# Kernel tuning notes

Measured on AMD Instinct MI355X. Metric: run time of the kernel, lower is better.

## Reference

```python
import jax, jax.numpy as jnp
import numpy as np

B, S, D = 4, 2048, 1024  # batch, seq_len, isize; FFN hidden = isize, gate dim = 2*isize


def setup_inputs() -> dict:
    key = jax.random.key(0)
    ks = jax.random.split(key, 6)
    sc = lambda n: 1.0 / np.sqrt(n)
    return {
        "iQ": jax.random.normal(ks[0], (B, S, D), jnp.float32),
        "iV": jax.random.normal(ks[1], (B, S, D), jnp.float32),
        "W1": jax.random.normal(ks[2], (D, D), jnp.float32) * sc(D),
        "b1": jnp.zeros((D,), jnp.float32),
        "W2": jax.random.normal(ks[3], (D, D), jnp.float32) * sc(D),
        "b2": jnp.zeros((D,), jnp.float32),
        "Wg": jax.random.normal(ks[4], (2 * D, 2 * D), jnp.float32) * sc(2 * D),
        "bg": jnp.zeros((2 * D,), jnp.float32),
    }


def reference(iQ, iV, W1, b1, W2, b2, Wg, bg):
    seql = iV.shape[1]
    # AAN cumulative-average matrix: row i has 1/(i+1) in cols 0..i (lower triangular)
    inv = 1.0 / jnp.arange(1, seql + 1, dtype=iV.dtype)  # [S]
    attn = jnp.tril(jnp.broadcast_to(inv[:, None], (seql, seql)))  # [S, S]
    avg = jnp.einsum('st,btd->bsd', attn, iV)  # [B, S, D]
    # PositionwiseFF with norm_input=False, dropout=0: Linear -> ReLU -> Linear
    h = jax.nn.relu(avg @ W1 + b1)
    ffn = h @ W2 + b2  # [B, S, D]
    # sigmoid gate over concat(iQ, ffn)
    g = jax.nn.sigmoid(jnp.concatenate([iQ, ffn], axis=-1) @ Wg + bg)  # [B, S, 2D]
    d = ffn.shape[-1]
    igate = g[..., :d]
    fgate = g[..., d:]
    return igate * iQ + fgate * ffn
```

## Files before the change

### kernel.cpp

```cpp
#include <hip/hip_runtime.h>
#include <hip/hip_bf16.h>
#include <cstdint>

typedef unsigned short u16;
typedef unsigned int   u32;

typedef __attribute__((ext_vector_type(8))) short short8;
typedef __attribute__((ext_vector_type(4))) float f32x4;

__device__ __forceinline__ float b2f(u16 v) { return __uint_as_float(((u32)v) << 16); }
__device__ __forceinline__ u16 f2b(float f) {
    u32 u = __float_as_uint(f);
    u += 0x7FFFu + ((u >> 16) & 1u);
    return (u16)(u >> 16);
}

#define G2L16(gp, lp) __builtin_amdgcn_global_load_lds(                       \
    (const __attribute__((address_space(1))) void*)(gp),                      \
    (__attribute__((address_space(3))) void*)(lp), 16, 0, 0)

__device__ __forceinline__ void transpose_body(const float* __restrict__ in,
                                               u16* __restrict__ out,
                                               int R, int C, int lb, int tilesX,
                                               float (*tile)[33]) {
    const int bx = (lb % tilesX) * 32;
    const int by = (lb / tilesX) * 32;
    const int tx = threadIdx.x & 31, ty = threadIdx.x >> 5;
    #pragma unroll
    for (int i = 0; i < 32; i += 8)
        tile[ty + i][tx] = in[(size_t)(by + ty + i) * C + (bx + tx)];
    __syncthreads();
    #pragma unroll
    for (int i = 0; i < 32; i += 8)
        out[(size_t)(bx + ty + i) * R + (by + tx)] = f2b(tile[tx][ty + i]);
}

__global__ void prologue_kernel(const float* __restrict__ W1, u16* __restrict__ W1t,
                                const float* __restrict__ W2, u16* __restrict__ W2t,
                                const float* __restrict__ Wg, u16* __restrict__ Wgt,
                                const float* __restrict__ iQ, u16* __restrict__ iQb,
                                const float* __restrict__ iV, float* __restrict__ csum) {
    __shared__ float tile[32][33];
    const int bid = blockIdx.x;
    const int tid = threadIdx.x;
    if (bid < 1024) {
        transpose_body(W1, W1t, 1024, 1024, bid, 32, tile);
    } else if (bid < 2048) {
        transpose_body(W2, W2t, 1024, 1024, bid - 1024, 32, tile);
    } else if (bid < 6144) {
        transpose_body(Wg, Wgt, 2048, 2048, bid - 2048, 64, tile);
    } else if (bid < 14336) {
        const size_t i = ((size_t)(bid - 6144) * 256 + tid) * 4;
        const float4 v = *(const float4*)(iQ + i);
        ushort4 o;
        o.x = f2b(v.x); o.y = f2b(v.y); o.z = f2b(v.z); o.w = f2b(v.w);
        *(ushort4*)(iQb + i) = o;
    } else {
        const int idx = bid - 14336;
        const int b = idx >> 6, c = idx & 63;
        const int d = tid * 4;
        const float* src = iV + ((size_t)(b * 2048 + c * 32)) * 1024 + d;
        float4 s = {0.f, 0.f, 0.f, 0.f};
        #pragma unroll 8
        for (int i = 0; i < 32; ++i) {
            const float4 v = *(const float4*)(src + (size_t)i * 1024);
            s.x += v.x; s.y += v.y; s.z += v.z; s.w += v.w;
        }
        *(float4*)(csum + ((size_t)(b * 64 + c)) * 1024 + d) = s;
    }
}

__global__ void scan_kernel(const float* __restrict__ iV, const float* __restrict__ csum,
                            u16* __restrict__ avg) {
    const int c = blockIdx.x & 63, b = blockIdx.x >> 6;
    const int d = threadIdx.x * 4;
    const float* cs = csum + (size_t)b * 64 * 1024 + d;
    float4 a0 = {0,0,0,0}, a1 = {0,0,0,0}, a2 = {0,0,0,0}, a3 = {0,0,0,0};
    int cc = 0;
    for (; cc + 4 <= c; cc += 4) {
        const float4 v0 = *(const float4*)(cs + (size_t)(cc + 0) * 1024);
        const float4 v1 = *(const float4*)(cs + (size_t)(cc + 1) * 1024);
        const float4 v2 = *(const float4*)(cs + (size_t)(cc + 2) * 1024);
        const float4 v3 = *(const float4*)(cs + (size_t)(cc + 3) * 1024);
        a0.x += v0.x; a0.y += v0.y; a0.z += v0.z; a0.w += v0.w;
        a1.x += v1.x; a1.y += v1.y; a1.z += v1.z; a1.w += v1.w;
        a2.x += v2.x; a2.y += v2.y; a2.z += v2.z; a2.w += v2.w;
        a3.x += v3.x; a3.y += v3.y; a3.z += v3.z; a3.w += v3.w;
    }
    for (; cc < c; ++cc) {
        const float4 v = *(const float4*)(cs + (size_t)cc * 1024);
        a0.x += v.x; a0.y += v.y; a0.z += v.z; a0.w += v.w;
    }
    float4 acc;
    acc.x = (a0.x + a1.x) + (a2.x + a3.x);
    acc.y = (a0.y + a1.y) + (a2.y + a3.y);
    acc.z = (a0.z + a1.z) + (a2.z + a3.z);
    acc.w = (a0.w + a1.w) + (a2.w + a3.w);

    const size_t off = ((size_t)(b * 2048 + c * 32)) * 1024 + d;
    const float* src = iV + off;
    u16*         dst = avg + off;
    const int s0 = c * 32;
    #pragma unroll 4
    for (int i = 0; i < 32; ++i) {
        const float4 v = *(const float4*)(src + (size_t)i * 1024);
        acc.x += v.x; acc.y += v.y; acc.z += v.z; acc.w += v.w;
        const float inv = 1.0f / (float)(s0 + i + 1);
        ushort4 o;
        o.x = f2b(acc.x * inv); o.y = f2b(acc.y * inv);
        o.z = f2b(acc.z * inv); o.w = f2b(acc.w * inv);
        *(ushort4*)(dst + (size_t)i * 1024) = o;
    }
}

template <int EPI>
__global__ __launch_bounds__(256, 2)
void gemm_kernel(const u16* __restrict__ A, const u16* __restrict__ Bt,
                 const float* __restrict__ bias, u16* __restrict__ C,
                 int M, int N, int K) {
    __shared__ u16 As[128 * 64];
    __shared__ u16 Bs[128 * 64];

    const int tid  = threadIdx.x;
    const int m0   = blockIdx.x * 128;
    const int n0   = blockIdx.y * 128;
    const int wave = tid >> 6, lane = tid & 63;
    const int wm   = (wave & 1) << 6;
    const int wn   = (wave >> 1) << 6;
    const int quad = lane >> 4, l16 = lane & 15;

    f32x4 acc[4][4];
    #pragma unroll
    for (int i = 0; i < 4; ++i)
        #pragma unroll
        for (int j = 0; j < 4; ++j) acc[i][j] = (f32x4){0.f, 0.f, 0.f, 0.f};

    int oo[4], rr[4], qq[4];
    #pragma unroll
    for (int j = 0; j < 4; ++j) {
        oo[j] = tid * 16 + j * 4096;
        rr[j] = oo[j] >> 7;
        qq[j] = ((oo[j] >> 4) & 7) ^ (rr[j] & 7);
    }

    const int ktiles = K >> 6;
    for (int kt = 0; kt < ktiles; ++kt) {
        const int kb = kt << 6;
        #pragma unroll
        for (int j = 0; j < 4; ++j) {
            G2L16((const char*)A  + ((size_t)(m0 + rr[j]) * K + kb) * 2 + qq[j] * 16,
                  (char*)As + oo[j]);
            G2L16((const char*)Bt + ((size_t)(n0 + rr[j]) * K + kb) * 2 + qq[j] * 16,
                  (char*)Bs + oo[j]);
        }
        __syncthreads();

        #pragma unroll
        for (int h = 0; h < 2; ++h) {
            short8 af[4], bf[4];
            #pragma unroll
            for (int mi = 0; mi < 4; ++mi) {
                const int R = wm + mi * 16 + l16;
                af[mi] = *(const short8*)(As + R * 64 + ((((h << 2) | quad) ^ (R & 7)) << 3));
            }
            #pragma unroll
            for (int ni = 0; ni < 4; ++ni) {
                const int R = wn + ni * 16 + l16;
                bf[ni] = *(const short8*)(Bs + R * 64 + ((((h << 2) | quad) ^ (R & 7)) << 3));
            }
            #pragma unroll
            for (int mi = 0; mi < 4; ++mi)
                #pragma unroll
                for (int ni = 0; ni < 4; ++ni)
                    acc[mi][ni] = __builtin_amdgcn_mfma_f32_16x16x32_bf16(
                        af[mi], bf[ni], acc[mi][ni], 0, 0, 0);
        }
        __syncthreads();
    }

    #pragma unroll
    for (int ni = 0; ni < 4; ++ni) {
        const int col = n0 + wn + ni * 16 + l16;
        const float bv = bias[col];
        #pragma unroll
        for (int mi = 0; mi < 4; ++mi) {
            const int row0 = m0 + wm + mi * 16 + quad * 4;
            #pragma unroll
            for (int r = 0; r < 4; ++r) {
                float v = acc[mi][ni][r] + bv;
                if (EPI == 0) v = fmaxf(v, 0.f);
                C[(size_t)(row0 + r) * N + col] = f2b(v);
            }
        }
    }
}

#define VM4  asm volatile("s_waitcnt vmcnt(4)" ::: "memory")
#define VM0  asm volatile("s_waitcnt vmcnt(0)" ::: "memory")
#define NOVM ((void)0)

#define SA(BUF, MH, T) do {                                                     \
    const char* b_ = ((T) < 16) ? ((const char*)iQb + (size_t)(T) * 128)        \
                                : ((const char*)ffn + (size_t)((T) - 16) * 128); \
    G2L16(b_ + gA[MH][0], (char*)&As[BUF][MH][0] + lo[0]);                      \
    G2L16(b_ + gA[MH][1], (char*)&As[BUF][MH][0] + lo[1]);                      \
  } while (0)

#define SB(BUF, GG, T) do {                                                     \
    const char* b_ = (const char*)Wgt + (size_t)(T) * 128;                      \
    G2L16(b_ + gB[GG][0], (char*)&Bs[BUF][GG][0] + lo[0]);                      \
    G2L16(b_ + gB[GG][1], (char*)&Bs[BUF][GG][0] + lo[1]);                      \
  } while (0)

#define PHASE(BUF, MH, G, STAGES, VMW) do {                                     \
    short8 af[4][2], bf[2][2];                                                  \
    {                                                                           \
      const char* Ab_ = (const char*)&As[BUF][MH][0];                           \
      const char* Bb_ = (const char*)&Bs[BUF][G][0];                            \
      _Pragma("unroll")                                                         \
      for (int mi = 0; mi < 4; ++mi) {                                          \
        af[mi][0] = *(const short8*)(Ab_ + aF[mi][0]);                          \
        af[mi][1] = *(const short8*)(Ab_ + aF[mi][1]);                          \
      }                                                                         \
      bf[0][0] = *(const short8*)(Bb_ + bF[0][0]);                              \
      bf[0][1] = *(const short8*)(Bb_ + bF[0][1]);                              \
      bf[1][0] = *(const short8*)(Bb_ + bF[1][0]);                              \
      bf[1][1] = *(const short8*)(Bb_ + bF[1][1]);                              \
    }                                                                           \
    STAGES                                                                      \
    __builtin_amdgcn_sched_barrier(0);                                          \
    __builtin_amdgcn_s_barrier();                                               \
    asm volatile("s_waitcnt lgkmcnt(0)" ::: "memory");                          \
    __builtin_amdgcn_sched_barrier(0);                                          \
    __builtin_amdgcn_s_setprio(1);                                              \
    _Pragma("unroll")                                                           \
    for (int mi = 0; mi < 4; ++mi) {                                            \
      _Pragma("unroll")                                                         \
      for (int ni = 0; ni < 2; ++ni) {                                          \
        acc[G][(MH) * 4 + mi][ni] = __builtin_amdgcn_mfma_f32_16x16x32_bf16(    \
            af[mi][0], bf[ni][0], acc[G][(MH) * 4 + mi][ni], 0, 0, 0);          \
        acc[G][(MH) * 4 + mi][ni] = __builtin_amdgcn_mfma_f32_16x16x32_bf16(    \
            af[mi][1], bf[ni][1], acc[G][(MH) * 4 + mi][ni], 0, 0, 0);          \
      }                                                                         \
    }                                                                           \
    __builtin_amdgcn_s_setprio(0);                                              \
    __builtin_amdgcn_sched_barrier(0);                                          \
    VMW;                                                                        \
    __builtin_amdgcn_s_barrier();                                               \
    __builtin_amdgcn_sched_barrier(0);                                          \
  } while (0)

__global__ __launch_bounds__(512, 2)
void gate8_kernel(const u16* __restrict__ iQb, const u16* __restrict__ ffn,
                  const u16* __restrict__ Wgt, const float* __restrict__ bg,
                  const float* __restrict__ iQ, float* __restrict__ out) {
    __shared__ u16 As[2][2][128 * 64];
    __shared__ u16 Bs[2][2][128 * 64];

    const int tid  = threadIdx.x;
    const int bid  = blockIdx.x;
    const int m0   = (bid & 31) * 256;
    const int n0   = (bid >> 5) * 128;
    const int wave = tid >> 6, lane = tid & 63;
    const int wm   = wave & 1;
    const int wn   = wave >> 1;
    const int quad = lane >> 4, l16 = lane & 15;

    u32 lo[2], gA[2][2], gB[2][2];
    #pragma unroll
    for (int j = 0; j < 2; ++j) {
        const u32 o = (u32)tid * 16 + (u32)j * 8192;
        const u32 r = o >> 7;
        const u32 q = ((o >> 4) & 7) ^ (r & 7);
        lo[j]    = o;
        gA[0][j] = (u32)(m0 + r) * 2048 + q * 16;
        gA[1][j] = (u32)(m0 + 128 + r) * 2048 + q * 16;
        gB[0][j] = (u32)(n0 + r) * 4096 + q * 16;
        gB[1][j] = (u32)(n0 + 1024 + r) * 4096 + q * 16;
    }

    u32 aF[4][2], bF[2][2];
    #pragma unroll
    for (int mi = 0; mi < 4; ++mi) {
        const int R = wm * 64 + mi * 16 + l16;
        #pragma unroll
        for (int ks = 0; ks < 2; ++ks)
            aF[mi][ks] = (u32)R * 128 + (u32)((((ks << 2) | quad) ^ (R & 7)) << 4);
    }
    #pragma unroll
    for (int ni = 0; ni < 2; ++ni) {
        const int R = wn * 32 + ni * 16 + l16;
        #pragma unroll
        for (int ks = 0; ks < 2; ++ks)
            bF[ni][ks] = (u32)R * 128 + (u32)((((ks << 2) | quad) ^ (R & 7)) << 4);
    }

    f32x4 acc[2][8][2];
    #pragma unroll
    for (int g = 0; g < 2; ++g)
        #pragma unroll
        for (int mf = 0; mf < 8; ++mf)
            #pragma unroll
            for (int ni = 0; ni < 2; ++ni)
                acc[g][mf][ni] = (f32x4){0.f, 0.f, 0.f, 0.f};

    SA(0, 0, 0); SA(0, 1, 0); SB(0, 0, 0); SB(0, 1, 0);
    SA(1, 0, 1); SB(1, 1, 1);
    VM4;
    __builtin_amdgcn_s_barrier();
    __builtin_amdgcn_sched_barrier(0);

    for (int i = 0; i < 15; ++i) {
        const int t0 = 2 * i, t1 = t0 + 1;
        PHASE(0, 0, 0, SA(1, 1, t1);     SB(1, 0, t1);     , NOVM);
        PHASE(0, 0, 1,                                     , NOVM);
        PHASE(0, 1, 1, SA(0, 0, t0 + 2);                   , NOVM);
        PHASE(0, 1, 0, SB(0, 1, t0 + 2);                   , VM4);
        PHASE(1, 0, 0, SB(0, 0, t0 + 2); SA(0, 1, t0 + 2); , NOVM);
        PHASE(1, 0, 1,                                     , NOVM);
        PHASE(1, 1, 1, SA(1, 0, t1 + 2);                   , NOVM);
        PHASE(1, 1, 0, SB(1, 1, t1 + 2);                   , VM4);
    }
    PHASE(0, 0, 0, SA(1, 1, 31); SB(1, 0, 31); , NOVM);
    PHASE(0, 0, 1,                             , NOVM);
    PHASE(0, 1, 1,                             , NOVM);
    PHASE(0, 1, 0,                             , VM0);
    PHASE(1, 0, 0,                             , NOVM);
    PHASE(1, 0, 1,                             , NOVM);
    PHASE(1, 1, 1,                             , NOVM);
    PHASE(1, 1, 0,                             , NOVM);

    #pragma unroll
    for (int ni = 0; ni < 2; ++ni) {
        const int col = n0 + wn * 32 + ni * 16 + l16;
        const float bgi = bg[col];
        const float bgf = bg[col + 1024];
        #pragma unroll
        for (int mh = 0; mh < 2; ++mh)
            #pragma unroll
            for (int mi = 0; mi < 4; ++mi) {
                const int row0 = m0 + mh * 128 + wm * 64 + mi * 16 + quad * 4;
                #pragma unroll
                for (int r = 0; r < 4; ++r) {
                    const size_t idx = (size_t)(row0 + r) * 1024 + col;
                    const float gi = 1.0f / (1.0f + __expf(-(acc[0][mh * 4 + mi][ni][r] + bgi)));
                    const float gf = 1.0f / (1.0f + __expf(-(acc[1][mh * 4 + mi][ni][r] + bgf)));
                    out[idx] = gi * iQ[idx] + gf * b2f(ffn[idx]);
                }
            }
    }
}

extern "C" void kernel_launch(void* const* d_in, const int* in_sizes, int n_in,
                              void* d_out, int out_size, void* d_ws, size_t ws_size,
                              hipStream_t stream) {
    const int B = 4, S = 2048, D = 1024, D2 = 2048;
    const int M = B * S;

    const float* iQ = (const float*)d_in[0];
    const float* iV = (const float*)d_in[1];
    const float* W1 = (const float*)d_in[2];
    const float* b1 = (const float*)d_in[3];
    const float* W2 = (const float*)d_in[4];
    const float* b2 = (const float*)d_in[5];
    const float* Wg = (const float*)d_in[6];
    const float* bg = (const float*)d_in[7];
    float* out = (float*)d_out;

    u16*   regA = (u16*)d_ws;
    u16*   regB = regA + (size_t)M * D;
    u16*   iQb  = regB + (size_t)M * D;
    u16*   W1t  = iQb  + (size_t)M * D;
    u16*   W2t  = W1t  + (size_t)D * D;
    u16*   Wgt  = W2t  + (size_t)D * D;
    float* csum = (float*)(Wgt + (size_t)D2 * D2);

    u16* avg = regA;
    u16* ffn = regA;
    u16* h   = regB;

    prologue_kernel<<<14592, 256, 0, stream>>>(W1, W1t, W2, W2t, Wg, Wgt,
                                               iQ, iQb, iV, csum);
    scan_kernel<<<B * 64, 256, 0, stream>>>(iV, csum, avg);
    gemm_kernel<0><<<dim3(M / 128, D / 128), 256, 0, stream>>>(avg, W1t, b1, h, M, D, D);
    gemm_kernel<1><<<dim3(M / 128, D / 128), 256, 0, stream>>>(h, W2t, b2, ffn, M, D, D);
    gate8_kernel<<<256, 512, 0, stream>>>(iQb, ffn, Wgt, bg, iQ, out);
}
```

Measured before the change: 284.4 us.

## Restructure gate GEMM into four phases with both B-halves kept in registers

```diff
diff --git a/kernel.cpp b/kernel.cpp
--- a/kernel.cpp
+++ b/kernel.cpp
@@ -212,20 +212,27 @@
     G2L16(b_ + gB[GG][1], (char*)&Bs[BUF][GG][0] + lo[1]);                      \
   } while (0)
 
-#define PHASE(BUF, MH, G, STAGES, VMW) do {                                     \
-    short8 af[4][2], bf[2][2];                                                  \
+#define PHASE(BUF, MH, RDB, STAGES, VMW) do {                                   \
+    short8 af[4][2];                                                            \
     {                                                                           \
       const char* Ab_ = (const char*)&As[BUF][MH][0];                           \
-      const char* Bb_ = (const char*)&Bs[BUF][G][0];                            \
       _Pragma("unroll")                                                         \
       for (int mi = 0; mi < 4; ++mi) {                                          \
         af[mi][0] = *(const short8*)(Ab_ + aF[mi][0]);                          \
         af[mi][1] = *(const short8*)(Ab_ + aF[mi][1]);                          \
       }                                                                         \
-      bf[0][0] = *(const short8*)(Bb_ + bF[0][0]);                              \
-      bf[0][1] = *(const short8*)(Bb_ + bF[0][1]);                              \
-      bf[1][0] = *(const short8*)(Bb_ + bF[1][0]);                              \
-      bf[1][1] = *(const short8*)(Bb_ + bF[1][1]);                              \
+      if (RDB) {                                                                \
+        const char* B0_ = (const char*)&Bs[BUF][0][0];                          \
+        const char* B1_ = (const char*)&Bs[BUF][1][0];                          \
+        _Pragma("unroll")                                                       \
+        for (int ni = 0; ni < 2; ++ni) {                                        \
+          _Pragma("unroll")                                                     \
+          for (int ks = 0; ks < 2; ++ks) {                                      \
+            bf[0][ni][ks] = *(const short8*)(B0_ + bF[ni][ks]);                 \
+            bf[1][ni][ks] = *(const short8*)(B1_ + bF[ni][ks]);                 \
+          }                                                                     \
+        }                                                                       \
+      }                                                                         \
     }                                                                           \
     STAGES                                                                      \
     __builtin_amdgcn_sched_barrier(0);                                          \
@@ -234,13 +241,16 @@
     __builtin_amdgcn_sched_barrier(0);                                          \
     __builtin_amdgcn_s_setprio(1);                                              \
     _Pragma("unroll")                                                           \
-    for (int mi = 0; mi < 4; ++mi) {                                            \
+    for (int ks = 0; ks < 2; ++ks) {                                            \
       _Pragma("unroll")                                                         \
-      for (int ni = 0; ni < 2; ++ni) {                                          \
-        acc[G][(MH) * 4 + mi][ni] = __builtin_amdgcn_mfma_f32_16x16x32_bf16(    \
-            af[mi][0], bf[ni][0], acc[G][(MH) * 4 + mi][ni], 0, 0, 0);          \
-        acc[G][(MH) * 4 + mi][ni] = __builtin_amdgcn_mfma_f32_16x16x32_bf16(    \
-            af[mi][1], bf[ni][1], acc[G][(MH) * 4 + mi][ni], 0, 0, 0);          \
+      for (int mi = 0; mi < 4; ++mi) {                                          \
+        _Pragma("unroll")                                                       \
+        for (int ni = 0; ni < 2; ++ni) {                                        \
+          acc[0][(MH) * 4 + mi][ni] = __builtin_amdgcn_mfma_f32_16x16x32_bf16(  \
+              af[mi][ks], bf[0][ni][ks], acc[0][(MH) * 4 + mi][ni], 0, 0, 0);   \
+          acc[1][(MH) * 4 + mi][ni] = __builtin_amdgcn_mfma_f32_16x16x32_bf16(  \
+              af[mi][ks], bf[1][ni][ks], acc[1][(MH) * 4 + mi][ni], 0, 0, 0);   \
+        }                                                                       \
       }                                                                         \
     }                                                                           \
     __builtin_amdgcn_s_setprio(0);                                              \
@@ -251,7 +261,7 @@
   } while (0)
 
 __global__ __launch_bounds__(512, 2)
-void gate8_kernel(const u16* __restrict__ iQb, const u16* __restrict__ ffn,
+void gate4_kernel(const u16* __restrict__ iQb, const u16* __restrict__ ffn,
                   const u16* __restrict__ Wgt, const float* __restrict__ bg,
                   const float* __restrict__ iQ, float* __restrict__ out) {
     __shared__ u16 As[2][2][128 * 64];
@@ -304,30 +314,24 @@
             for (int ni = 0; ni < 2; ++ni)
                 acc[g][mf][ni] = (f32x4){0.f, 0.f, 0.f, 0.f};
 
+    short8 bf[2][2][2];
+
     SA(0, 0, 0); SA(0, 1, 0); SB(0, 0, 0); SB(0, 1, 0);
-    SA(1, 0, 1); SB(1, 1, 1);
+    SA(1, 0, 1); SB(1, 0, 1);
     VM4;
     __builtin_amdgcn_s_barrier();
     __builtin_amdgcn_sched_barrier(0);
 
     for (int i = 0; i < 15; ++i) {
         const int t0 = 2 * i, t1 = t0 + 1;
-        PHASE(0, 0, 0, SA(1, 1, t1);     SB(1, 0, t1);     , NOVM);
-        PHASE(0, 0, 1,                                     , NOVM);
-        PHASE(0, 1, 1, SA(0, 0, t0 + 2);                   , NOVM);
-        PHASE(0, 1, 0, SB(0, 1, t0 + 2);                   , VM4);
-        PHASE(1, 0, 0, SB(0, 0, t0 + 2); SA(0, 1, t0 + 2); , NOVM);
-        PHASE(1, 0, 1,                                     , NOVM);
-        PHASE(1, 1, 1, SA(1, 0, t1 + 2);                   , NOVM);
-        PHASE(1, 1, 0, SB(1, 1, t1 + 2);                   , VM4);
-    }
-    PHASE(0, 0, 0, SA(1, 1, 31); SB(1, 0, 31); , NOVM);
-    PHASE(0, 0, 1,                             , NOVM);
-    PHASE(0, 1, 1,                             , NOVM);
+        PHASE(0, 0, 1, SA(1, 1, t1);     SB(1, 1, t1);     , NOVM);
+        PHASE(0, 1, 0, SA(0, 0, t0 + 2); SB(0, 0, t0 + 2); , VM4);
+        PHASE(1, 0, 1, SB(0, 1, t0 + 2); SA(0, 1, t0 + 2); , NOVM);
+        PHASE(1, 1, 0, SA(1, 0, t1 + 2); SB(1, 0, t1 + 2); , VM4);
+    }
+    PHASE(0, 0, 1, SA(1, 1, 31); SB(1, 1, 31); , NOVM);
     PHASE(0, 1, 0,                             , VM0);
-    PHASE(1, 0, 0,                             , NOVM);
     PHASE(1, 0, 1,                             , NOVM);
-    PHASE(1, 1, 1,                             , NOVM);
     PHASE(1, 1, 0,                             , NOVM);
 
     #pragma unroll
@@ -384,5 +388,5 @@
     scan_kernel<<<B * 64, 256, 0, stream>>>(iV, csum, avg);
     gemm_kernel<0><<<dim3(M / 128, D / 128), 256, 0, stream>>>(avg, W1t, b1, h, M, D, D);
     gemm_kernel<1><<<dim3(M / 128, D / 128), 256, 0, stream>>>(h, W2t, b2, ffn, M, D, D);
-    gate8_kernel<<<256, 512, 0, stream>>>(iQb, ffn, Wgt, bg, iQ, out);
-}
+    gate4_kernel<<<256, 512, 0, stream>>>(iQb, ffn, Wgt, bg, iQ, out);
+}
```

After: 276.5 us. -2.8%, faster.
